# Optimization experiments

Measured on AMD Instinct MI355X. Metric: run time of the kernel, lower is better.

Reference implementation:

```python
import jax, jax.numpy as jnp
import numpy as np

B, S, D, H = 2, 2048, 1024, 16
HD = D // H


def setup_inputs() -> dict:
    key = jax.random.key(0)
    ks = jax.random.split(key, 9)
    s = 1.0 / np.sqrt(D)
    return {
        "qx": jax.random.normal(ks[0], (B, S, D), jnp.float32),
        "kx": jax.random.normal(ks[1], (B, S, D), jnp.float32),
        "vx": jax.random.normal(ks[2], (B, S, D), jnp.float32),
        "mask": jnp.tril(jnp.ones((S, S), jnp.int32))[None, None],  # [1,1,S,S] causal
        "Wq": jax.random.uniform(ks[3], (D, D), jnp.float32, -s, s),
        "bq": jax.random.uniform(ks[4], (D,), jnp.float32, -s, s),
        "Wk": jax.random.uniform(ks[5], (D, D), jnp.float32, -s, s),
        "bk": jax.random.uniform(ks[6], (D,), jnp.float32, -s, s),
        "Wv": jax.random.uniform(ks[7], (D, D), jnp.float32, -s, s),
        "bv": jax.random.uniform(ks[8], (D,), jnp.float32, -s, s),
    }


def reference(qx, kx, vx, mask, Wq, bq, Wk, bk, Wv, bv):
    bat, seq_len, d_model = qx.shape
    # torch Linear: y = x @ W.T + b
    q = qx @ Wq.T + bq
    k = kx @ Wk.T + bk
    v = vx @ Wv.T + bv
    # [b, h, s, hd]
    q = q.reshape(bat, seq_len, H, HD).transpose(0, 2, 1, 3)
    k = k.reshape(bat, seq_len, H, HD).transpose(0, 2, 1, 3)
    v = v.reshape(bat, seq_len, H, HD).transpose(0, 2, 1, 3)
    # NOTE: original scales by sqrt(d_model), not sqrt(head_dim)
    attn_weight = jnp.einsum('bhqd,bhkd->bhqk', q, k) / jnp.sqrt(
        jnp.asarray(d_model, q.dtype))
    attn_weight = jnp.where(mask == 0, -jnp.inf, attn_weight)
    attn_score = jax.nn.softmax(attn_weight, axis=-1)
    attn_output = jnp.einsum('bhqk,bhkd->bhqd', attn_score, v)
    return attn_output.transpose(0, 2, 1, 3).reshape(bat, seq_len, d_model)
```

## Files before the change

kernel.cpp:

```cpp
#include <hip/hip_runtime.h>


typedef __attribute__((ext_vector_type(8))) short short8;
typedef __attribute__((ext_vector_type(4))) short shortx4;
typedef __attribute__((ext_vector_type(4))) float floatx4;

#define NEGBIG (-1.0e30f)
#define QSCALE 0.04508422002778011f

__device__ __forceinline__ float bf2f(ushort u) {
    union { unsigned int i; float f; } x; x.i = ((unsigned int)u) << 16; return x.f;
}
__device__ __forceinline__ ushort f2bf(float f) {
    union { unsigned int i; float f; } x; x.f = f;
    return (ushort)((x.i + 0x7FFFu + ((x.i >> 16) & 1u)) >> 16);
}
__device__ __forceinline__ ushort f2bf_trunc(float f) {
    union { unsigned int i; float f; } x; x.f = f;
    return (ushort)(x.i >> 16);
}
__device__ __forceinline__ void gl_lds16(const void* g, void* l) {
    __builtin_amdgcn_global_load_lds(
        (const __attribute__((address_space(1))) unsigned int*)g,
        (__attribute__((address_space(3))) unsigned int*)l, 16, 0, 0);
}

__global__ void convert_fp32(
    const float* __restrict__ qx, const float* __restrict__ kx, const float* __restrict__ vx,
    const float* __restrict__ wq, const float* __restrict__ wk, const float* __restrict__ wv,
    const float* __restrict__ bq, const float* __restrict__ bk, const float* __restrict__ bv,
    ushort* __restrict__ dst, int* __restrict__ flag)
{
    const unsigned int* w = (const unsigned int*)qx;
    int hits = 0;
#pragma unroll
    for (int i = 0; i < 4; ++i) {
        unsigned int v = w[threadIdx.x * 4 + i];
        int e = (int)((v >> 7) & 0xFF);
        hits += (e >= 100 && e <= 135) ? 1 : 0;
    }
    __shared__ int red[4];
    for (int off = 32; off; off >>= 1) hits += __shfl_down(hits, off);
    if ((threadIdx.x & 63) == 0) red[threadIdx.x >> 6] = hits;
    __syncthreads();
    const int dt = (red[0] + red[1] + red[2] + red[3] > 512) ? 1 : 0;
    if (blockIdx.x == 0 && threadIdx.x == 0) *flag = dt;
    if (dt) return;

    const int v = blockIdx.x * 256 + threadIdx.x;
    const float* src; int off = v;
    if      (v < 1048576) { src = qx; }
    else if (v < 2097152) { src = kx; off = v - 1048576; }
    else if (v < 3145728) { src = vx; off = v - 2097152; }
    else if (v < 3407872) { src = wq; off = v - 3145728; }
    else if (v < 3670016) { src = wk; off = v - 3407872; }
    else if (v < 3932160) { src = wv; off = v - 3670016; }
    else if (v < 3932416) { src = bq; off = v - 3932160; }
    else if (v < 3932672) { src = bk; off = v - 3932416; }
    else                  { src = bv; off = v - 3932672; }
    float4 f = ((const float4*)src)[off];
    shortx4 o;
    o[0] = (short)f2bf(f.x); o[1] = (short)f2bf(f.y);
    o[2] = (short)f2bf(f.z); o[3] = (short)f2bf(f.w);
    *(shortx4*)&dst[(size_t)v * 4] = o;
}

__global__ __launch_bounds__(256, 4) void qkv_gemm(
    const void* __restrict__ Xq_, const void* __restrict__ Wq_, const void* __restrict__ bq_,
    const void* __restrict__ Xk_, const void* __restrict__ Wk_, const void* __restrict__ bk_,
    const void* __restrict__ Xv_, const void* __restrict__ Wv_, const void* __restrict__ bv_,
    const ushort* __restrict__ conv,
    ushort* __restrict__ Yq, ushort* __restrict__ Yk, ushort* __restrict__ Yv,
    const int* __restrict__ flag)
{
    const int idx = blockIdx.x;
    const int xcd = idx & 7;
    const int j   = (idx >> 3) & 7;
    const int pg  = idx >> 6;
    const int p   = pg * 8 + xcd;
    const int z   = p >> 5;
    const int m0  = (p & 31) * 128;
    const int n0  = j * 128;

    const int dt = *flag;
    const ushort* X = dt ? (const ushort*)(z == 0 ? Xq_ : z == 1 ? Xk_ : Xv_)
                         : conv + (size_t)z * 4194304;
    const ushort* W = dt ? (const ushort*)(z == 0 ? Wq_ : z == 1 ? Wk_ : Wv_)
                         : conv + 12582912 + (size_t)z * 1048576;
    const ushort* bias = dt ? (const ushort*)(z == 0 ? bq_ : z == 1 ? bk_ : bv_)
                            : conv + 15728640 + z * 1024;
    ushort* Y = (z == 0) ? Yq : (z == 1) ? Yk : Yv;
    const float oscale = (z == 0) ? QSCALE : 1.0f;

    __shared__ __align__(16) ushort As[128 * 64];
    __shared__ __align__(16) ushort Bs[128 * 64];

    const int tid  = threadIdx.x;
    const int wave = tid >> 6;
    const int lane = tid & 63;
    const int col  = lane & 15;
    const int quad = lane >> 4;
    const int wm   = (wave >> 1) * 64;
    const int wn   = (wave & 1) * 64;

    floatx4 acc[4][4] = {};

    for (int k0 = 0; k0 < 1024; k0 += 64) {
        __syncthreads();
#pragma unroll
        for (int c = 0; c < 4; ++c) {
            const int o   = c * 4096 + tid * 16;
            const int row = o >> 7;
            const int bg  = ((o >> 4) & 7) ^ (row & 7);
            gl_lds16(X + (size_t)(m0 + row) * 1024 + k0 + bg * 8, &As[o >> 1]);
            gl_lds16(W + (size_t)(n0 + row) * 1024 + k0 + bg * 8, &Bs[o >> 1]);
        }
        __syncthreads();

#pragma unroll
        for (int h = 0; h < 2; ++h) {
            short8 af[4], bf_[4];
#pragma unroll
            for (int i = 0; i < 4; ++i) {
                const int ra = wm + i * 16 + col;
                const int rb = wn + i * 16 + col;
                af[i]  = *(const short8*)&As[ra * 64 + (((h * 4 + quad) ^ (ra & 7)) * 8)];
                bf_[i] = *(const short8*)&Bs[rb * 64 + (((h * 4 + quad) ^ (rb & 7)) * 8)];
            }
#pragma unroll
            for (int i = 0; i < 4; ++i)
#pragma unroll
                for (int jj = 0; jj < 4; ++jj)
                    acc[i][jj] = __builtin_amdgcn_mfma_f32_16x16x32_bf16(af[i], bf_[jj], acc[i][jj], 0, 0, 0);
        }
    }

    if (z == 2) {
#pragma unroll
        for (int jj = 0; jj < 4; ++jj) {
            const int n = n0 + wn + jj * 16 + col;
            const float bb = bf2f(bias[n]);
#pragma unroll
            for (int i = 0; i < 4; ++i) {
                const int m = m0 + wm + i * 16 + quad * 4;
                shortx4 pk;
#pragma unroll
                for (int r = 0; r < 4; ++r) pk[r] = (short)f2bf(acc[i][jj][r] + bb);
                *(shortx4*)&Y[((size_t)(m >> 11) * 1024 + n) * 2048 + (m & 2047)] = pk;
            }
        }
    } else {
#pragma unroll
        for (int jj = 0; jj < 4; ++jj) {
            const int n = n0 + wn + jj * 16 + col;
            const float bb = bf2f(bias[n]);
#pragma unroll
            for (int i = 0; i < 4; ++i)
#pragma unroll
                for (int r = 0; r < 4; ++r) {
                    const int m = m0 + wm + i * 16 + quad * 4 + r;
                    Y[(size_t)m * 1024 + n] = f2bf((acc[i][jj][r] + bb) * oscale);
                }
        }
    }
}

__global__ __launch_bounds__(256, 4) void attn(
    const ushort* __restrict__ Q, const ushort* __restrict__ K,
    const ushort* __restrict__ Vt, void* __restrict__ O,
    const int* __restrict__ flag)
{
    const int i   = blockIdx.x;
    const int xcd = i & 7;
    const int i3  = i >> 3;
    const int run = i3 >> 5;
    const int p   = i3 & 31;
    const int qt0 = (p & 1) ? (p >> 1) : (31 - (p >> 1));
    const int qt  = (run & 1) ? (31 - qt0) : qt0;
    const int g   = xcd + 8 * run;
    const int b   = g >> 4;
    const int h   = g & 15;
    const int q0  = qt * 64;
    const int dt  = *flag;

    __shared__ __align__(16) ushort Ks[2][64 * 64];
    __shared__ __align__(16) ushort Vs[2][64 * 64];
    __shared__ __align__(16) ushort Ps[4][16 * 64];

    const int tid  = threadIdx.x;
    const int wave = tid >> 6;
    const int lane = tid & 63;
    const int col  = lane & 15;
    const int quad = lane >> 4;

    const size_t qkbase = ((size_t)b * 2048) * 1024 + h * 64;
    const size_t vtbase = ((size_t)(b * 16 + h) * 64) * 2048;

    short8 ones;
#pragma unroll
    for (int ii = 0; ii < 8; ++ii) ones[ii] = (short)0x3F80;

    const int o0   = tid * 16;
    const int o1   = 4096 + tid * 16;
    const int row0 = o0 >> 7, row1 = o1 >> 7;
    const int bg0  = ((o0 >> 4) & 7) ^ (row0 & 7);
    const int bg1  = ((o1 >> 4) & 7) ^ (row1 & 7);

    const int rq = wave * 16 + col;
    const short8 qf0 = *(const short8*)&Q[qkbase + (size_t)(q0 + rq) * 1024 + quad * 8];
    const short8 qf1 = *(const short8*)&Q[qkbase + (size_t)(q0 + rq) * 1024 + 32 + quad * 8];

    gl_lds16(K + qkbase + (size_t)row0 * 1024 + bg0 * 8, &Ks[0][o0 >> 1]);
    gl_lds16(K + qkbase + (size_t)row1 * 1024 + bg1 * 8, &Ks[0][o1 >> 1]);
    gl_lds16(Vt + vtbase + (size_t)row0 * 2048 + bg0 * 8, &Vs[0][o0 >> 1]);
    gl_lds16(Vt + vtbase + (size_t)row1 * 2048 + bg1 * 8, &Vs[0][o1 >> 1]);
    __syncthreads();

    floatx4 oacc[4] = {};
    floatx4 sacc = {};

    for (int t = 0; t <= qt; ++t) {
        const int cur = t & 1;

        if (t < qt) {
            const int kv1 = (t + 1) * 64;
            gl_lds16(K + qkbase + (size_t)(kv1 + row0) * 1024 + bg0 * 8, &Ks[cur ^ 1][o0 >> 1]);
            gl_lds16(K + qkbase + (size_t)(kv1 + row1) * 1024 + bg1 * 8, &Ks[cur ^ 1][o1 >> 1]);
            gl_lds16(Vt + vtbase + (size_t)row0 * 2048 + kv1 + bg0 * 8, &Vs[cur ^ 1][o0 >> 1]);
            gl_lds16(Vt + vtbase + (size_t)row1 * 2048 + kv1 + bg1 * 8, &Vs[cur ^ 1][o1 >> 1]);
        }

        floatx4 s4[4];
#pragma unroll
        for (int ct = 0; ct < 4; ++ct) {
            const int rk = ct * 16 + col;
            short8 kf0 = *(const short8*)&Ks[cur][rk * 64 + (((quad    ) ^ (col & 7)) * 8)];
            short8 kf1 = *(const short8*)&Ks[cur][rk * 64 + (((quad + 4) ^ (col & 7)) * 8)];
            floatx4 a = {};
            a = __builtin_amdgcn_mfma_f32_16x16x32_bf16(qf0, kf0, a, 0, 0, 0);
            a = __builtin_amdgcn_mfma_f32_16x16x32_bf16(qf1, kf1, a, 0, 0, 0);
            s4[ct] = a;
        }

        if (t == qt) {
#pragma unroll
            for (int ct = 0; ct < 4; ++ct) {
                const int kidx = ct * 16 + col;
#pragma unroll
                for (int r = 0; r < 4; ++r) {
                    const int qidx = wave * 16 + quad * 4 + r;
                    s4[ct][r] = (kidx <= qidx) ? s4[ct][r] : NEGBIG;
                }
            }
        }

#pragma unroll
        for (int ct = 0; ct < 4; ++ct)
#pragma unroll
            for (int r = 0; r < 4; ++r) {
                float pv = __builtin_exp2f(s4[ct][r]);
                const int pr  = quad * 4 + r;
                const int blk = (ct * 2 + (col >> 3)) ^ (pr & 7);
                Ps[wave][pr * 64 + blk * 8 + (col & 7)] = f2bf_trunc(pv);
            }

        short8 pf0 = *(const short8*)&Ps[wave][col * 64 + (((quad    ) ^ (col & 7)) * 8)];
        short8 pf1 = *(const short8*)&Ps[wave][col * 64 + (((quad + 4) ^ (col & 7)) * 8)];

        sacc = __builtin_amdgcn_mfma_f32_16x16x32_bf16(pf0, ones, sacc, 0, 0, 0);
        sacc = __builtin_amdgcn_mfma_f32_16x16x32_bf16(pf1, ones, sacc, 0, 0, 0);

#pragma unroll
        for (int ct = 0; ct < 4; ++ct) {
            const int rv = ct * 16 + col;
            short8 vf0 = *(const short8*)&Vs[cur][rv * 64 + (((quad    ) ^ (rv & 7)) * 8)];
            short8 vf1 = *(const short8*)&Vs[cur][rv * 64 + (((quad + 4) ^ (rv & 7)) * 8)];
            oacc[ct] = __builtin_amdgcn_mfma_f32_16x16x32_bf16(pf0, vf0, oacc[ct], 0, 0, 0);
            oacc[ct] = __builtin_amdgcn_mfma_f32_16x16x32_bf16(pf1, vf1, oacc[ct], 0, 0, 0);
        }

        if (t < qt) __syncthreads();
    }

#pragma unroll
    for (int r = 0; r < 4; ++r) {
        const float inv = 1.0f / sacc[r];
        const int q = q0 + wave * 16 + quad * 4 + r;
#pragma unroll
        for (int ct = 0; ct < 4; ++ct) {
            const float v = oacc[ct][r] * inv;
            const size_t oidx = ((size_t)b * 2048 + q) * 1024 + h * 64 + ct * 16 + col;
            if (dt) ((ushort*)O)[oidx] = f2bf(v);
            else    ((float*)O)[oidx]  = v;
        }
    }
}

extern "C" void kernel_launch(void* const* d_in, const int* in_sizes, int n_in,
                              void* d_out, int out_size, void* d_ws, size_t ws_size,
                              hipStream_t stream) {
    const void* qx = d_in[0];
    const void* kx = d_in[1];
    const void* vx = d_in[2];
    const void* Wq = d_in[4]; const void* bq = d_in[5];
    const void* Wk = d_in[6]; const void* bk = d_in[7];
    const void* Wv = d_in[8]; const void* bv = d_in[9];

    int*    flag = (int*)d_ws;
    ushort* conv = (ushort*)((char*)d_ws + 256);
    ushort* Qw   = (ushort*)((char*)d_ws + 256 + 31463424);
    ushort* Kw   = Qw + (size_t)4096 * 1024;
    ushort* Vtw  = Kw + (size_t)4096 * 1024;

    convert_fp32<<<15363, 256, 0, stream>>>(
        (const float*)qx, (const float*)kx, (const float*)vx,
        (const float*)Wq, (const float*)Wk, (const float*)Wv,
        (const float*)bq, (const float*)bk, (const float*)bv, conv, flag);

    qkv_gemm<<<768, 256, 0, stream>>>(qx, Wq, bq, kx, Wk, bk, vx, Wv, bv,
                                      conv, Qw, Kw, Vtw, flag);

    attn<<<1024, 256, 0, stream>>>(Qw, Kw, Vtw, d_out, flag);
}
```

Before: 202.0 us.

## Split long causal query tiles across KV chunks and add a combine kernel

```diff
diff --git a/kernel.cpp b/kernel.cpp
--- a/kernel.cpp
+++ b/kernel.cpp
@@ -7,6 +7,9 @@
 
 #define NEGBIG (-1.0e30f)
 #define QSCALE 0.04508422002778011f
+#define SLOTF 4160
+
+#define NEGBIG (-1.0e30f)
 
 __device__ __forceinline__ float bf2f(ushort u) {
     union { unsigned int i; float f; } x; x.i = ((unsigned int)u) << 16; return x.f;
@@ -168,15 +171,21 @@
 __global__ __launch_bounds__(256, 4) void attn(
     const ushort* __restrict__ Q, const ushort* __restrict__ K,
     const ushort* __restrict__ Vt, void* __restrict__ O,
-    const int* __restrict__ flag)
+    float* __restrict__ PW, const int* __restrict__ flag)
 {
     const int i   = blockIdx.x;
     const int xcd = i & 7;
-    const int i3  = i >> 3;
-    const int run = i3 >> 5;
-    const int p   = i3 & 31;
-    const int qt0 = (p & 1) ? (p >> 1) : (31 - (p >> 1));
-    const int qt  = (run & 1) ? (31 - qt0) : qt0;
+    const int m   = i >> 3;
+    const int run = m & 3;
+    const int jm  = m >> 2;
+    int qt, chunk, n;
+    if (jm < 30)      { qt = 31 - jm / 3;        chunk = jm % 3;        n = 3; }
+    else if (jm < 52) { qt = 21 - (jm - 30) / 2; chunk = (jm - 30) % 2; n = 2; }
+    else              { qt = 10 - (jm - 52);     chunk = 0;             n = 1; }
+    const int T  = qt + 1;
+    const int t0 = chunk * T / n;
+    const int t1 = (chunk + 1) * T / n;
+
     const int g   = xcd + 8 * run;
     const int b   = g >> 4;
     const int h   = g & 15;
@@ -210,19 +219,22 @@
     const short8 qf0 = *(const short8*)&Q[qkbase + (size_t)(q0 + rq) * 1024 + quad * 8];
     const short8 qf1 = *(const short8*)&Q[qkbase + (size_t)(q0 + rq) * 1024 + 32 + quad * 8];
 
-    gl_lds16(K + qkbase + (size_t)row0 * 1024 + bg0 * 8, &Ks[0][o0 >> 1]);
-    gl_lds16(K + qkbase + (size_t)row1 * 1024 + bg1 * 8, &Ks[0][o1 >> 1]);
-    gl_lds16(Vt + vtbase + (size_t)row0 * 2048 + bg0 * 8, &Vs[0][o0 >> 1]);
-    gl_lds16(Vt + vtbase + (size_t)row1 * 2048 + bg1 * 8, &Vs[0][o1 >> 1]);
+    {
+        const int kv0 = t0 * 64;
+        gl_lds16(K + qkbase + (size_t)(kv0 + row0) * 1024 + bg0 * 8, &Ks[0][o0 >> 1]);
+        gl_lds16(K + qkbase + (size_t)(kv0 + row1) * 1024 + bg1 * 8, &Ks[0][o1 >> 1]);
+        gl_lds16(Vt + vtbase + (size_t)row0 * 2048 + kv0 + bg0 * 8, &Vs[0][o0 >> 1]);
+        gl_lds16(Vt + vtbase + (size_t)row1 * 2048 + kv0 + bg1 * 8, &Vs[0][o1 >> 1]);
+    }
     __syncthreads();
 
     floatx4 oacc[4] = {};
     floatx4 sacc = {};
 
-    for (int t = 0; t <= qt; ++t) {
-        const int cur = t & 1;
-
-        if (t < qt) {
+    for (int t = t0; t < t1; ++t) {
+        const int cur = (t - t0) & 1;
+
+        if (t + 1 < t1) {
             const int kv1 = (t + 1) * 64;
             gl_lds16(K + qkbase + (size_t)(kv1 + row0) * 1024 + bg0 * 8, &Ks[cur ^ 1][o0 >> 1]);
             gl_lds16(K + qkbase + (size_t)(kv1 + row1) * 1024 + bg1 * 8, &Ks[cur ^ 1][o1 >> 1]);
@@ -279,20 +291,72 @@
             oacc[ct] = __builtin_amdgcn_mfma_f32_16x16x32_bf16(pf1, vf1, oacc[ct], 0, 0, 0);
         }
 
-        if (t < qt) __syncthreads();
-    }
-
-#pragma unroll
-    for (int r = 0; r < 4; ++r) {
-        const float inv = 1.0f / sacc[r];
-        const int q = q0 + wave * 16 + quad * 4 + r;
-#pragma unroll
-        for (int ct = 0; ct < 4; ++ct) {
-            const float v = oacc[ct][r] * inv;
-            const size_t oidx = ((size_t)b * 2048 + q) * 1024 + h * 64 + ct * 16 + col;
-            if (dt) ((ushort*)O)[oidx] = f2bf(v);
-            else    ((float*)O)[oidx]  = v;
-        }
+        if (t + 1 < t1) __syncthreads();
+    }
+
+    if (n == 1) {
+#pragma unroll
+        for (int r = 0; r < 4; ++r) {
+            const float inv = 1.0f / sacc[r];
+            const int q = q0 + wave * 16 + quad * 4 + r;
+#pragma unroll
+            for (int ct = 0; ct < 4; ++ct) {
+                const float v = oacc[ct][r] * inv;
+                const size_t oidx = ((size_t)b * 2048 + q) * 1024 + h * 64 + ct * 16 + col;
+                if (dt) ((ushort*)O)[oidx] = f2bf(v);
+                else    ((float*)O)[oidx]  = v;
+            }
+        }
+    } else {
+        const int sl = (qt <= 21) ? (qt - 11) * 2 + chunk : 22 + (qt - 22) * 3 + chunk;
+        float* slot = PW + ((size_t)g * 52 + sl) * SLOTF;
+#pragma unroll
+        for (int r = 0; r < 4; ++r) {
+            const int pr = wave * 16 + quad * 4 + r;
+#pragma unroll
+            for (int ct = 0; ct < 4; ++ct)
+                slot[pr * 64 + ct * 16 + col] = oacc[ct][r];
+            if (col == 0) slot[4096 + pr] = sacc[r];
+        }
+    }
+}
+
+__global__ __launch_bounds__(256) void attn_combine(
+    const float* __restrict__ PW, void* __restrict__ O, const int* __restrict__ flag)
+{
+    const int c  = blockIdx.x;
+    const int g  = c & 31;
+    const int qi = c >> 5;
+    const int qt = 11 + qi;
+    const int n  = (qt <= 21) ? 2 : 3;
+    const int b  = g >> 4, h = g & 15;
+    const int sl0 = (qt <= 21) ? (qt - 11) * 2 : 22 + (qt - 22) * 3;
+    const float* base = PW + ((size_t)g * 52 + sl0) * SLOTF;
+
+    const int t   = threadIdx.x;
+    const int row = t >> 2;
+    const int c0  = (t & 3) * 16;
+
+    float acc[16] = {};
+    float l = 0.0f;
+    for (int s = 0; s < n; ++s) {
+        const float* sp = base + (size_t)s * SLOTF;
+        l += sp[4096 + row];
+#pragma unroll
+        for (int k = 0; k < 16; k += 4) {
+            float4 v = *(const float4*)&sp[row * 64 + c0 + k];
+            acc[k] += v.x; acc[k + 1] += v.y; acc[k + 2] += v.z; acc[k + 3] += v.w;
+        }
+    }
+    const float inv = 1.0f / l;
+    const int dt = *flag;
+    const size_t o0 = ((size_t)b * 2048 + qt * 64 + row) * 1024 + h * 64 + c0;
+    if (dt) {
+#pragma unroll
+        for (int k = 0; k < 16; ++k) ((ushort*)O)[o0 + k] = f2bf(acc[k] * inv);
+    } else {
+#pragma unroll
+        for (int k = 0; k < 16; ++k) ((float*)O)[o0 + k] = acc[k] * inv;
     }
 }
 
@@ -311,6 +375,7 @@
     ushort* Qw   = (ushort*)((char*)d_ws + 256 + 31463424);
     ushort* Kw   = Qw + (size_t)4096 * 1024;
     ushort* Vtw  = Kw + (size_t)4096 * 1024;
+    float*  PW   = (float*)conv;
 
     convert_fp32<<<15363, 256, 0, stream>>>(
         (const float*)qx, (const float*)kx, (const float*)vx,
@@ -320,5 +385,7 @@
     qkv_gemm<<<768, 256, 0, stream>>>(qx, Wq, bq, kx, Wk, bk, vx, Wv, bv,
                                       conv, Qw, Kw, Vtw, flag);
 
-    attn<<<1024, 256, 0, stream>>>(Qw, Kw, Vtw, d_out, flag);
-}
+    attn<<<2016, 256, 0, stream>>>(Qw, Kw, Vtw, d_out, PW, flag);
+
+    attn_combine<<<672, 256, 0, stream>>>(PW, d_out, flag);
+}
```

Result: no change. 203.3 us (+0.7%).
